# Optimization experiments

Measured on AMD Instinct MI355X. Metric: run time of the kernel, lower is better.

## Reference

```python
import jax, jax.numpy as jnp
import numpy as np

E, H, F, N, B = 512, 8, 2048, 1024, 4
HD = E // H


def setup_inputs() -> dict:
    key = jax.random.key(0)
    ks = jax.random.split(key, 20)
    s = 0.02
    return {
        "node_inputs": jax.random.normal(ks[0], (N, B, E), jnp.float32),
        "parent_mask": jax.random.uniform(ks[1], (B, N, N), jnp.float32),
        "hidden": jax.random.bernoulli(ks[2], 0.5, (B, N, N)),
        "pad_mask": jax.random.bernoulli(ks[3], 0.1, (B, N)),
        "Wp": jax.random.normal(ks[4], (H, E), jnp.float32) * s,
        "bp": jnp.zeros((H,), jnp.float32),
        "Wc": jax.random.normal(ks[5], (H, E), jnp.float32) * s,
        "bc": jnp.zeros((H,), jnp.float32),
        "Wqkv": jax.random.normal(ks[6], (3 * E, E), jnp.float32) * s,
        "bqkv": jnp.zeros((3 * E,), jnp.float32),
        "Wo": jax.random.normal(ks[7], (E, E), jnp.float32) * s,
        "bo": jnp.zeros((E,), jnp.float32),
        "W1": jax.random.normal(ks[8], (F, E), jnp.float32) * s,
        "b1": jnp.zeros((F,), jnp.float32),
        "W2": jax.random.normal(ks[9], (E, F), jnp.float32) * s,
        "b2": jnp.zeros((E,), jnp.float32),
        "ln1_g": jnp.ones((E,), jnp.float32),
        "ln1_b": jnp.zeros((E,), jnp.float32),
        "ln2_g": jnp.ones((E,), jnp.float32),
        "ln2_b": jnp.zeros((E,), jnp.float32),
    }


def _layer_norm(x, g, b, eps=1e-5):
    m = jnp.mean(x, axis=-1, keepdims=True)
    v = jnp.mean((x - m) ** 2, axis=-1, keepdims=True)
    return (x - m) * jax.lax.rsqrt(v + eps) * g + b


def reference(node_inputs, parent_mask, hidden, pad_mask, Wp, bp, Wc, bc,
              Wqkv, bqkv, Wo, bo, W1, b1, W2, b2, ln1_g, ln1_b, ln2_g, ln2_b):
    x = node_inputs  # (N, B, E), seq-first like nn.TransformerEncoderLayer
    # parent/child per-head biases: Linear(E->H), permuted to (B, H, N)
    pbias = jnp.transpose(x @ Wp.T + bp, (1, 2, 0))
    cbias = jnp.transpose(x @ Wc.T + bc, (1, 2, 0))
    # additive attention bias (B, H, N, N)
    am = (jnp.swapaxes(parent_mask, 1, 2)[:, None] * pbias[..., None]
          + parent_mask[:, None] * cbias[..., None])
    am = jnp.where(hidden[:, None], -jnp.inf, am)
    # multi-head self-attention
    qkv = x @ Wqkv.T + bqkv  # (N, B, 3E)
    q, k, v = jnp.split(qkv, 3, axis=-1)

    def heads(t):  # (N, B, E) -> (B, H, N, HD)
        return jnp.transpose(t.reshape(N, B, H, HD), (1, 2, 0, 3))

    q, k, v = heads(q), heads(k), heads(v)
    scores = jnp.einsum("bhqd,bhkd->bhqk", q, k) / jnp.sqrt(jnp.float32(HD)) + am
    scores = jnp.where(pad_mask[:, None, None, :], -jnp.inf, scores)
    attn = jax.nn.softmax(scores, axis=-1)
    ctx = jnp.einsum("bhqk,bhkd->bhqd", attn, v)  # (B, H, N, HD)
    ctx = jnp.transpose(ctx, (2, 0, 1, 3)).reshape(N, B, E)
    attn_out = ctx @ Wo.T + bo
    # post-norm transformer encoder layer (dropout=0, relu activation)
    y = _layer_norm(x + attn_out, ln1_g, ln1_b)
    ff = jax.nn.relu(y @ W1.T + b1) @ W2.T + b2
    return _layer_norm(y + ff, ln2_g, ln2_b)
```

## Files before the change

### kernel.cpp

```cpp
#include <hip/hip_runtime.h>
#include <hip/hip_bf16.h>
#include <stdint.h>

using bf16 = __hip_bfloat16;

typedef __bf16 bf16x8 __attribute__((ext_vector_type(8)));
typedef float  f32x4  __attribute__((ext_vector_type(4)));

__device__ __forceinline__ float bflo(uint32_t u) { return __uint_as_float(u << 16); }
__device__ __forceinline__ float bfhi(uint32_t u) { return __uint_as_float(u & 0xffff0000u); }

__device__ __forceinline__ void load8(const bf16* p, float* f) {
  uint4 u = *(const uint4*)p;
  f[0] = bflo(u.x); f[1] = bfhi(u.x);
  f[2] = bflo(u.y); f[3] = bfhi(u.y);
  f[4] = bflo(u.z); f[5] = bfhi(u.z);
  f[6] = bflo(u.w); f[7] = bfhi(u.w);
}
__device__ __forceinline__ void load8(const float* p, float* f) {
  float4 a = *(const float4*)p, b = *(const float4*)(p + 4);
  f[0] = a.x; f[1] = a.y; f[2] = a.z; f[3] = a.w;
  f[4] = b.x; f[5] = b.y; f[6] = b.z; f[7] = b.w;
}
__device__ __forceinline__ void store1(float* o, float v) { *o = v; }
__device__ __forceinline__ void store1(bf16* o, float v) { *o = __float2bfloat16(v); }
__device__ __forceinline__ uint32_t bfbits(float x) {
  bf16 v = __float2bfloat16(x);
  return (uint32_t)*(uint16_t*)&v;
}

typedef const uint32_t __attribute__((address_space(1)))* gp_t;
typedef uint32_t __attribute__((address_space(3)))* lp_t;
__device__ __forceinline__ void gload16(const void* g, void* l) {
  __builtin_amdgcn_global_load_lds((gp_t)g, (lp_t)l, 16, 0, 0);
}

__global__ __launch_bounds__(256)
void prologue(const float* __restrict__ pm, const int* __restrict__ hid,
              const int* __restrict__ padm, uint32_t* __restrict__ mout,
              const float* __restrict__ x, const float* __restrict__ Wqkv,
              const float* __restrict__ Wo, const float* __restrict__ W1,
              const float* __restrict__ W2, bf16* __restrict__ xb,
              bf16* __restrict__ wq, bf16* __restrict__ wob,
              bf16* __restrict__ w1b, bf16* __restrict__ w2b,
              const float* __restrict__ bqkv, const float* __restrict__ bp,
              const float* __restrict__ bc, const float* __restrict__ Wp,
              const float* __restrict__ Wc, float* __restrict__ bias_ext)
{
  __shared__ float tileT[128][65];
  const int blk = blockIdx.x, t = threadIdx.x;
  if (blk < 512) {
    const int k0 = (blk & 7) * 128, q0 = ((blk >> 3) & 15) * 64, b = blk >> 7;
    const size_t pb = (size_t)b << 20;
#pragma unroll
    for (int i = 0; i < 32; ++i) {
      int idx = t + i * 256;
      int r = idx >> 6, c = idx & 63;
      tileT[r][c] = pm[pb + (size_t)(k0 + r) * 1024 + q0 + c];
    }
    __syncthreads();
#pragma unroll
    for (int i = 0; i < 32; ++i) {
      int idx = t + i * 256;
      int q = idx >> 7, k = idx & 127;
      size_t src = pb + (size_t)(q0 + q) * 1024 + k0 + k;
      int msk = hid[src] | padm[b * 1024 + k0 + k];
      uint32_t u = 0xFFFFFFFFu;
      if (!msk) u = (bfbits(tileT[k][q]) << 16) | bfbits(pm[src]);
      mout[src] = u;
    }
  } else if (blk < 3072) {
    size_t j = ((size_t)(blk - 512) * 256 + t) * 8;
    const float* s; bf16* o; size_t off;
    if      (j < 2097152) { s = x;    o = xb;  off = j; }
    else if (j < 2883584) { s = Wqkv; o = wq;  off = j - 2097152; }
    else if (j < 3145728) { s = Wo;   o = wob; off = j - 2883584; }
    else if (j < 4194304) { s = W1;   o = w1b; off = j - 3145728; }
    else                  { s = W2;   o = w2b; off = j - 4194304; }
    float f[8];
    load8(s + off, f);
    uint4 u;
    u.x = (bfbits(f[1]) << 16) | bfbits(f[0]);
    u.y = (bfbits(f[3]) << 16) | bfbits(f[2]);
    u.z = (bfbits(f[5]) << 16) | bfbits(f[4]);
    u.w = (bfbits(f[7]) << 16) | bfbits(f[6]);
    *(uint4*)(o + off) = u;
  } else {
    int sb = blk - 3072;
    if (sb < 2) {
      int j = (sb * 256 + t) * 8;
      if (j < 4096) {
        float f[8]; load8(Wp + j, f);
#pragma unroll
        for (int i = 0; i < 8; ++i) wq[(size_t)1536 * 512 + j + i] = __float2bfloat16(f[i]);
      }
    } else if (sb < 4) {
      int j = ((sb - 2) * 256 + t) * 8;
      if (j < 4096) {
        float f[8]; load8(Wc + j, f);
#pragma unroll
        for (int i = 0; i < 8; ++i) wq[(size_t)1544 * 512 + j + i] = __float2bfloat16(f[i]);
      }
    } else {
      int j = t * 8;
#pragma unroll
      for (int i = 0; i < 8; ++i) {
        int cc = j + i;
        if (cc < 1664) {
          float v = 0.f;
          if (cc < 1536) v = bqkv[cc];
          else if (cc < 1544) v = bp[cc - 1536];
          else if (cc < 1552) v = bc[cc - 1544];
          bias_ext[cc] = v;
        }
      }
    }
  }
}

template<int MODE, int BN>
__global__ __launch_bounds__(256)
void gemm_bt(const bf16* __restrict__ A, const bf16* __restrict__ W,
             const float* __restrict__ bias, bf16* __restrict__ outb,
             float* __restrict__ outf, int M, int Nout, int K, int kLen)
{
  constexpr int NT = BN / 32;
  __shared__ bf16 As[128 * 64];
  __shared__ bf16 Bs[BN * 64];
  const int t = threadIdx.x, lane = t & 63, wave = t >> 6;
  const int m0 = blockIdx.y * 128, n0 = blockIdx.x * BN;
  const int kOff = blockIdx.z * kLen;
  if (MODE == 3) outf += (size_t)blockIdx.z * M * Nout;
  const int wr = wave >> 1, wc = wave & 1;
  const int frow = lane & 15, ksel = (lane >> 4) * 8;
  f32x4 acc[4 * NT] = {};
  const bf16* Ab = A + (size_t)m0 * K;
  const bf16* Wb = W + (size_t)n0 * K;

  for (int k0 = kOff; k0 < kOff + kLen; k0 += 64) {
    __syncthreads();
#pragma unroll
    for (int i = 0; i < 4; ++i) {
      int ib = i * 256 + wave * 64;
      int idx = ib + lane;
      gload16(Ab + (size_t)(idx >> 3) * K + k0 + (idx & 7) * 8, As + ib * 8);
    }
#pragma unroll
    for (int i = 0; i < BN / 32; ++i) {
      int ib = i * 256 + wave * 64;
      int idx = ib + lane;
      gload16(Wb + (size_t)(idx >> 3) * K + k0 + (idx & 7) * 8, Bs + ib * 8);
    }
    __syncthreads();
#pragma unroll
    for (int kk = 0; kk < 64; kk += 32) {
      bf16x8 af[4], bf_[NT];
#pragma unroll
      for (int mt = 0; mt < 4; ++mt)
        af[mt] = *(const bf16x8*)(As + (wr * 64 + mt * 16 + frow) * 64 + kk + ksel);
#pragma unroll
      for (int nt = 0; nt < NT; ++nt)
        bf_[nt] = *(const bf16x8*)(Bs + (wc * (BN / 2) + nt * 16 + frow) * 64 + kk + ksel);
#pragma unroll
      for (int mt = 0; mt < 4; ++mt)
#pragma unroll
        for (int nt = 0; nt < NT; ++nt)
          acc[mt * NT + nt] = __builtin_amdgcn_mfma_f32_16x16x32_bf16(
              af[mt], bf_[nt], acc[mt * NT + nt], 0, 0, 0);
    }
  }
  const int rb = (lane >> 4) * 4, cb = lane & 15;
#pragma unroll
  for (int mt = 0; mt < 4; ++mt)
#pragma unroll
    for (int nt = 0; nt < NT; ++nt) {
      f32x4 a = acc[mt * NT + nt];
#pragma unroll
      for (int r = 0; r < 4; ++r) {
        int row = m0 + wr * 64 + mt * 16 + rb + r;
        int col = n0 + wc * (BN / 2) + nt * 16 + cb;
        if (MODE == 3) {
          outf[(size_t)row * Nout + col] = a[r];
        } else {
          float v = a[r] + bias[col];
          if (MODE == 1) v = fmaxf(v, 0.f);
          if (MODE == 2) {
            if (col >= 1552) continue;
            int n = row >> 2, b = row & 3;
            if (col >= 1536) {
              int j = col - 1536;
              int hh = j & 7;
              outf[(j < 8 ? 0 : 32768) + (b * 8 + hh) * 1024 + n] = v;
            } else {
              int which = col >> 9, hh = (col >> 6) & 7, d = col & 63;
              if (which == 0) v *= 0.125f;
              size_t idx;
              if (which == 2)
                idx = (((size_t)(64 + b * 8 + hh)) << 16) + (size_t)d * 1024 + n;
              else
                idx = (((size_t)(which * 32 + b * 8 + hh)) << 16) + (size_t)n * 64 + d;
              outb[idx] = __float2bfloat16(v);
            }
          } else {
            outb[(size_t)row * Nout + col] = __float2bfloat16(v);
          }
        }
      }
    }
}

__global__ __launch_bounds__(256, 3)
void attn_mfma(const bf16* __restrict__ qkv, const float* __restrict__ pbw,
               const float* __restrict__ cbw, const uint32_t* __restrict__ mpk,
               bf16* __restrict__ opart, float2* __restrict__ mlout)
{
  __shared__ bf16 Kt[128 * 64];
  __shared__ bf16 Vt[64 * 128];
  __shared__ bf16 Ps[4][16][136];
  const int t = threadIdx.x, lane = t & 63, wave = t >> 6;
  const int g = lane >> 4, c = lane & 15;
  const int h = blockIdx.y, b = blockIdx.z >> 1, half = blockIdx.z & 1;
  const int q0 = blockIdx.x * 64 + wave * 16;
  const size_t bh = (size_t)b * 8 + h;
  const bf16* Qp = qkv + (bh << 16);
  const bf16* Kp = qkv + ((32 + bh) << 16);
  const bf16* Vg = qkv + ((64 + bh) << 16);

  bf16x8 qa0 = *(const bf16x8*)(Qp + (size_t)(q0 + c) * 64 + g * 8);
  bf16x8 qa1 = *(const bf16x8*)(Qp + (size_t)(q0 + c) * 64 + 32 + g * 8);

  const float pbq = pbw[bh * 1024 + q0 + c];
  const float cbq = cbw[bh * 1024 + q0 + c];
  const uint32_t* mrp = mpk + (((size_t)b * 1024 + q0 + c) << 10);

  f32x4 oacc[4] = {{0,0,0,0},{0,0,0,0},{0,0,0,0},{0,0,0,0}};
  float m = -1e30f, l = 0.f;

  for (int kt = 0; kt < 4; ++kt) {
    const int k0 = half * 512 + kt * 128;
    __syncthreads();
#pragma unroll
    for (int i = 0; i < 4; ++i) {
      int ib = i * 256 + wave * 64;
      int idx = ib + lane;
      int r = idx >> 3, p = idx & 7;
      gload16(Kp + (size_t)(k0 + r) * 64 + ((p ^ (r & 7)) * 8), Kt + ib * 8);
    }
#pragma unroll
    for (int i = 0; i < 4; ++i) {
      int ib = i * 256 + wave * 64;
      int idx = ib + lane;
      int d = idx >> 4, p = idx & 15;
      gload16(Vg + (size_t)d * 1024 + k0 + ((p ^ (d & 15)) * 8), Vt + ib * 8);
    }
    uint4 mu[8];
#pragma unroll
    for (int nt = 0; nt < 8; ++nt)
      mu[nt] = *(const uint4*)(mrp + k0 + nt * 16 + 4 * g);
    __syncthreads();
    f32x4 sacc[8];
#pragma unroll
    for (int nt = 0; nt < 8; ++nt) {
      f32x4 z = {0.f,0.f,0.f,0.f};
      int r = nt * 16 + c;
      bf16x8 k0f = *(const bf16x8*)(Kt + r * 64 + (( g      ^ (c & 7)) * 8));
      bf16x8 k1f = *(const bf16x8*)(Kt + r * 64 + (((4 + g) ^ (c & 7)) * 8));
      z = __builtin_amdgcn_mfma_f32_16x16x32_bf16(k0f, qa0, z, 0, 0, 0);
      z = __builtin_amdgcn_mfma_f32_16x16x32_bf16(k1f, qa1, z, 0, 0, 0);
      sacc[nt] = z;
    }
    float mx = -1e30f;
#pragma unroll
    for (int nt = 0; nt < 8; ++nt) {
      uint32_t uu[4] = {mu[nt].x, mu[nt].y, mu[nt].z, mu[nt].w};
#pragma unroll
      for (int r = 0; r < 4; ++r) {
        float s = sacc[nt][r] + bfhi(uu[r]) * pbq + bflo(uu[r]) * cbq;
        s = (uu[r] == 0xFFFFFFFFu) ? -1e30f : s;
        sacc[nt][r] = s;
        mx = fmaxf(mx, s);
      }
    }
    mx = fmaxf(mx, __shfl_xor(mx, 16));
    mx = fmaxf(mx, __shfl_xor(mx, 32));
    const float newm = fmaxf(m, mx);
    const float al = __expf(m - newm);
    float ps = 0.f;
#pragma unroll
    for (int nt = 0; nt < 8; ++nt) {
      float p0 = (sacc[nt][0] <= -1e29f) ? 0.f : __expf(sacc[nt][0] - newm);
      float p1 = (sacc[nt][1] <= -1e29f) ? 0.f : __expf(sacc[nt][1] - newm);
      float p2 = (sacc[nt][2] <= -1e29f) ? 0.f : __expf(sacc[nt][2] - newm);
      float p3 = (sacc[nt][3] <= -1e29f) ? 0.f : __expf(sacc[nt][3] - newm);
      ps += (p0 + p1) + (p2 + p3);
      uint2 w;
      w.x = (bfbits(p1) << 16) | bfbits(p0);
      w.y = (bfbits(p3) << 16) | bfbits(p2);
      *(uint2*)&Ps[wave][c][nt * 16 + 4 * g] = w;
    }
    ps += __shfl_xor(ps, 16);
    ps += __shfl_xor(ps, 32);
    l = l * al + ps;
    m = newm;
#pragma unroll
    for (int dt = 0; dt < 4; ++dt) {
      oacc[dt][0] *= al; oacc[dt][1] *= al;
      oacc[dt][2] *= al; oacc[dt][3] *= al;
    }
#pragma unroll
    for (int dt = 0; dt < 4; ++dt) {
      int row = dt * 16 + c;
#pragma unroll
      for (int kc = 0; kc < 4; ++kc) {
        bf16x8 vf = *(const bf16x8*)(Vt + row * 128 + (((kc * 4 + g) ^ c) * 8));
        bf16x8 pf = *(const bf16x8*)&Ps[wave][c][kc * 32 + g * 8];
        oacc[dt] = __builtin_amdgcn_mfma_f32_16x16x32_bf16(vf, pf, oacc[dt], 0, 0, 0);
      }
    }
  }
  const int qg = q0 + c;
  const size_t prow = ((size_t)(half * 32) + bh) * 1024 + qg;
#pragma unroll
  for (int dt = 0; dt < 4; ++dt)
#pragma unroll
    for (int rg = 0; rg < 4; ++rg)
      opart[prow * 64 + dt * 16 + 4 * g + rg] = __float2bfloat16(oacc[dt][rg]);
  if (g == 0) mlout[prow] = make_float2(m, l);
}

__global__ __launch_bounds__(256)
void attn_reduce(const bf16* __restrict__ opart, const float2* __restrict__ ml,
                 bf16* __restrict__ ctxo)
{
  const int idx = blockIdx.x * 256 + threadIdx.x;
  const int row = idx >> 3, seg = (idx & 7) * 8;
  float o0[8], o1[8];
  load8(opart + (size_t)row * 64 + seg, o0);
  load8(opart + (size_t)(row + 32768) * 64 + seg, o1);
  const float2 ml0 = ml[row], ml1 = ml[row + 32768];
  const float mst = fmaxf(ml0.x, ml1.x);
  const float w0 = __expf(ml0.x - mst), w1 = __expf(ml1.x - mst);
  const float denom = ml0.y * w0 + ml1.y * w1;
  const float inv = (denom > 0.f) ? 1.f / denom : 0.f;
  const int bh = row >> 10, q = row & 1023;
  const int b = bh >> 3, h = bh & 7;
  bf16* out = ctxo + ((size_t)q * 4 + b) * 512 + h * 64 + seg;
#pragma unroll
  for (int j = 0; j < 8; ++j)
    out[j] = __float2bfloat16((o0[j] * w0 + o1[j] * w1) * inv);
}

template<typename TA, typename TO>
__global__ __launch_bounds__(256)
void ln_res2(const TA* __restrict__ a, const float* __restrict__ p0,
             const float* __restrict__ p1, const float* __restrict__ bias,
             const float* __restrict__ g, const float* __restrict__ be,
             TO* __restrict__ out)
{
  const int wave = threadIdx.x >> 6, lane = threadIdx.x & 63;
  const int m = blockIdx.x * 4 + wave;
  const size_t base = (size_t)m * 512 + lane * 8;
  float va[8], f0[8], f1[8], bb[8];
  load8(a + base, va);
  load8(p0 + base, f0);
  load8(p1 + base, f1);
  load8(bias + lane * 8, bb);
  float v[8], s = 0.f;
#pragma unroll
  for (int j = 0; j < 8; ++j) { v[j] = va[j] + f0[j] + f1[j] + bb[j]; s += v[j]; }
#pragma unroll
  for (int off = 32; off; off >>= 1) s += __shfl_xor(s, off);
  const float mean = s * (1.f / 512.f);
  float q = 0.f;
#pragma unroll
  for (int j = 0; j < 8; ++j) { float d = v[j] - mean; q += d * d; }
#pragma unroll
  for (int off = 32; off; off >>= 1) q += __shfl_xor(q, off);
  const float rs = rsqrtf(q * (1.f / 512.f) + 1e-5f);
  float gv[8], bv[8];
  load8(g + lane * 8, gv);
  load8(be + lane * 8, bv);
#pragma unroll
  for (int j = 0; j < 8; ++j)
    store1(out + base + j, (v[j] - mean) * rs * gv[j] + bv[j]);
}

extern "C" void kernel_launch(void* const* d_in, const int* in_sizes, int n_in,
                              void* d_out, int out_size, void* d_ws, size_t ws_size,
                              hipStream_t stream)
{
  (void)in_sizes; (void)n_in; (void)out_size; (void)ws_size;
  const float* x    = (const float*)d_in[0];
  const float* pm   = (const float*)d_in[1];
  const int*   hid  = (const int*)d_in[2];
  const int*   padm = (const int*)d_in[3];
  const float* Wp   = (const float*)d_in[4];
  const float* bp   = (const float*)d_in[5];
  const float* Wc   = (const float*)d_in[6];
  const float* bc   = (const float*)d_in[7];
  const float* Wqkv = (const float*)d_in[8];
  const float* bqkv = (const float*)d_in[9];
  const float* Wo   = (const float*)d_in[10];
  const float* bo   = (const float*)d_in[11];
  const float* W1   = (const float*)d_in[12];
  const float* b1   = (const float*)d_in[13];
  const float* W2   = (const float*)d_in[14];
  const float* b2   = (const float*)d_in[15];
  const float* g1   = (const float*)d_in[16];
  const float* be1  = (const float*)d_in[17];
  const float* g2   = (const float*)d_in[18];
  const float* be2  = (const float*)d_in[19];

  char* ws = (char*)d_ws;
  bf16*     qkvb  = (bf16*)    (ws);
  float*    pbo   = (float*)   (ws + 12582912);
  float*    cbo   = (float*)   (ws + 12713984);
  uint32_t* mpk   = (uint32_t*)(ws + 12845056);
  bf16*     ctx   = (bf16*)    (ws + 29622272);
  float*    part  = (float*)   (ws);
  bf16*     ff1   = (bf16*)    (ws + 16777216);
  bf16*     y     = (bf16*)    (ws + 33816576);
  bf16*     xb    = (bf16*)    (ws + 38010880);
  bf16*     wqkvb = (bf16*)    (ws + 42205184);
  bf16*     wob   = (bf16*)    (ws + 43909120);
  bf16*     w1b   = (bf16*)    (ws + 44433408);
  bf16*     w2b   = (bf16*)    (ws + 46530560);
  float*    bext  = (float*)   (ws + 48627712);
  bf16*     opart = (bf16*)    (ws + 48634368);
  float2*   mlb   = (float2*)  (ws + 57022976);
  float*    part1 = part + (size_t)4096 * 512;

  prologue<<<3077, 256, 0, stream>>>(pm, hid, padm, mpk, x, Wqkv, Wo, W1, W2,
                                     xb, wqkvb, wob, w1b, w2b,
                                     bqkv, bp, bc, Wp, Wc, bext);
  gemm_bt<2, 128><<<dim3(13, 32), 256, 0, stream>>>(xb, wqkvb, bext, qkvb, pbo, 4096, 1664, 512, 512);
  attn_mfma<<<dim3(16, 8, 8), 256, 0, stream>>>(qkvb, pbo, cbo, mpk, opart, mlb);
  attn_reduce<<<1024, 256, 0, stream>>>(opart, mlb, ctx);
  gemm_bt<3, 64><<<dim3(8, 32, 2), 256, 0, stream>>>(ctx, wob, nullptr, nullptr, part, 4096, 512, 512, 256);
  ln_res2<float, bf16><<<1024, 256, 0, stream>>>(x, part, part1, bo, g1, be1, y);
  gemm_bt<1, 128><<<dim3(16, 32), 256, 0, stream>>>(y, w1b, b1, ff1, nullptr, 4096, 2048, 512, 512);
  gemm_bt<3, 64><<<dim3(8, 32, 2), 256, 0, stream>>>(ff1, w2b, nullptr, nullptr, part, 4096, 512, 2048, 1024);
  ln_res2<bf16, float><<<1024, 256, 0, stream>>>(y, part, part1, b2, g2, be2, (float*)d_out);
}
```

Baseline: 272.0 us.

## Co-schedule mask packing with QKV GEMM in one heterogeneous kernel

Moves the parent-mask transpose and pack work out of the prologue into a combined kernel with the QKV projection GEMM. Blocks 0-415 run the GEMM and the remaining 512 blocks build the packed mask. The aim is to overlap the memory-bound mask pass with the compute-bound GEMM, so neither leaves the GPU idle on its own. This adds a shared-memory union and a larger per-block footprint, which may lower GEMM occupancy.

```diff
diff --git a/kernel.cpp b/kernel.cpp
--- a/kernel.cpp
+++ b/kernel.cpp
@@ -36,9 +36,7 @@
 }
 
 __global__ __launch_bounds__(256)
-void prologue(const float* __restrict__ pm, const int* __restrict__ hid,
-              const int* __restrict__ padm, uint32_t* __restrict__ mout,
-              const float* __restrict__ x, const float* __restrict__ Wqkv,
+void cvt_prep(const float* __restrict__ x, const float* __restrict__ Wqkv,
               const float* __restrict__ Wo, const float* __restrict__ W1,
               const float* __restrict__ W2, bf16* __restrict__ xb,
               bf16* __restrict__ wq, bf16* __restrict__ wob,
@@ -47,30 +45,9 @@
               const float* __restrict__ bc, const float* __restrict__ Wp,
               const float* __restrict__ Wc, float* __restrict__ bias_ext)
 {
-  __shared__ float tileT[128][65];
   const int blk = blockIdx.x, t = threadIdx.x;
-  if (blk < 512) {
-    const int k0 = (blk & 7) * 128, q0 = ((blk >> 3) & 15) * 64, b = blk >> 7;
-    const size_t pb = (size_t)b << 20;
-#pragma unroll
-    for (int i = 0; i < 32; ++i) {
-      int idx = t + i * 256;
-      int r = idx >> 6, c = idx & 63;
-      tileT[r][c] = pm[pb + (size_t)(k0 + r) * 1024 + q0 + c];
-    }
-    __syncthreads();
-#pragma unroll
-    for (int i = 0; i < 32; ++i) {
-      int idx = t + i * 256;
-      int q = idx >> 7, k = idx & 127;
-      size_t src = pb + (size_t)(q0 + q) * 1024 + k0 + k;
-      int msk = hid[src] | padm[b * 1024 + k0 + k];
-      uint32_t u = 0xFFFFFFFFu;
-      if (!msk) u = (bfbits(tileT[k][q]) << 16) | bfbits(pm[src]);
-      mout[src] = u;
-    }
-  } else if (blk < 3072) {
-    size_t j = ((size_t)(blk - 512) * 256 + t) * 8;
+  if (blk < 2560) {
+    size_t j = ((size_t)blk * 256 + t) * 8;
     const float* s; bf16* o; size_t off;
     if      (j < 2097152) { s = x;    o = xb;  off = j; }
     else if (j < 2883584) { s = Wqkv; o = wq;  off = j - 2097152; }
@@ -86,7 +63,7 @@
     u.w = (bfbits(f[7]) << 16) | bfbits(f[6]);
     *(uint4*)(o + off) = u;
   } else {
-    int sb = blk - 3072;
+    int sb = blk - 2560;
     if (sb < 2) {
       int j = (sb * 256 + t) * 8;
       if (j < 4096) {
@@ -114,6 +91,111 @@
           bias_ext[cc] = v;
         }
       }
+    }
+  }
+}
+
+__global__ __launch_bounds__(256)
+void qkv_mask(const bf16* __restrict__ A, const bf16* __restrict__ W,
+              const float* __restrict__ bias, bf16* __restrict__ outb,
+              float* __restrict__ outf,
+              const float* __restrict__ pm, const int* __restrict__ hid,
+              const int* __restrict__ padm, uint32_t* __restrict__ mout)
+{
+  __shared__ char smem[33280];
+  const int blk = blockIdx.x, t = threadIdx.x;
+  if (blk < 416) {
+    bf16* As = (bf16*)smem;
+    bf16* Bs = (bf16*)(smem + 16384);
+    const int lane = t & 63, wave = t >> 6;
+    const int m0 = (blk / 13) * 128, n0 = (blk % 13) * 128;
+    const int wr = wave >> 1, wc = wave & 1;
+    const int frow = lane & 15, ksel = (lane >> 4) * 8;
+    f32x4 acc[16] = {};
+    const bf16* Ab = A + (size_t)m0 * 512;
+    const bf16* Wb = W + (size_t)n0 * 512;
+    for (int k0 = 0; k0 < 512; k0 += 64) {
+      __syncthreads();
+#pragma unroll
+      for (int i = 0; i < 4; ++i) {
+        int ib = i * 256 + wave * 64;
+        int idx = ib + lane;
+        gload16(Ab + (size_t)(idx >> 3) * 512 + k0 + (idx & 7) * 8, As + ib * 8);
+      }
+#pragma unroll
+      for (int i = 0; i < 4; ++i) {
+        int ib = i * 256 + wave * 64;
+        int idx = ib + lane;
+        gload16(Wb + (size_t)(idx >> 3) * 512 + k0 + (idx & 7) * 8, Bs + ib * 8);
+      }
+      __syncthreads();
+#pragma unroll
+      for (int kk = 0; kk < 64; kk += 32) {
+        bf16x8 af[4], bf_[4];
+#pragma unroll
+        for (int mt = 0; mt < 4; ++mt)
+          af[mt] = *(const bf16x8*)(As + (wr * 64 + mt * 16 + frow) * 64 + kk + ksel);
+#pragma unroll
+        for (int nt = 0; nt < 4; ++nt)
+          bf_[nt] = *(const bf16x8*)(Bs + (wc * 64 + nt * 16 + frow) * 64 + kk + ksel);
+#pragma unroll
+        for (int mt = 0; mt < 4; ++mt)
+#pragma unroll
+          for (int nt = 0; nt < 4; ++nt)
+            acc[mt * 4 + nt] = __builtin_amdgcn_mfma_f32_16x16x32_bf16(
+                af[mt], bf_[nt], acc[mt * 4 + nt], 0, 0, 0);
+      }
+    }
+    const int rb = (lane >> 4) * 4, cb = lane & 15;
+#pragma unroll
+    for (int mt = 0; mt < 4; ++mt)
+#pragma unroll
+      for (int nt = 0; nt < 4; ++nt) {
+        f32x4 a = acc[mt * 4 + nt];
+#pragma unroll
+        for (int r = 0; r < 4; ++r) {
+          int row = m0 + wr * 64 + mt * 16 + rb + r;
+          int col = n0 + wc * 64 + nt * 16 + cb;
+          if (col >= 1552) continue;
+          float v = a[r] + bias[col];
+          int n = row >> 2, b = row & 3;
+          if (col >= 1536) {
+            int j = col - 1536;
+            int hh = j & 7;
+            outf[(j < 8 ? 0 : 32768) + (b * 8 + hh) * 1024 + n] = v;
+          } else {
+            int which = col >> 9, hh = (col >> 6) & 7, d = col & 63;
+            if (which == 0) v *= 0.125f;
+            size_t idx;
+            if (which == 2)
+              idx = (((size_t)(64 + b * 8 + hh)) << 16) + (size_t)d * 1024 + n;
+            else
+              idx = (((size_t)(which * 32 + b * 8 + hh)) << 16) + (size_t)n * 64 + d;
+            outb[idx] = __float2bfloat16(v);
+          }
+        }
+      }
+  } else {
+    float (*tileT)[65] = (float(*)[65])smem;
+    const int mb = blk - 416;
+    const int k0 = (mb & 7) * 128, q0 = ((mb >> 3) & 15) * 64, b = mb >> 7;
+    const size_t pb = (size_t)b << 20;
+#pragma unroll
+    for (int i = 0; i < 32; ++i) {
+      int idx = t + i * 256;
+      int r = idx >> 6, c = idx & 63;
+      tileT[r][c] = pm[pb + (size_t)(k0 + r) * 1024 + q0 + c];
+    }
+    __syncthreads();
+#pragma unroll
+    for (int i = 0; i < 32; ++i) {
+      int idx = t + i * 256;
+      int q = idx >> 7, k = idx & 127;
+      size_t src = pb + (size_t)(q0 + q) * 1024 + k0 + k;
+      int msk = hid[src] | padm[b * 1024 + k0 + k];
+      uint32_t u = 0xFFFFFFFFu;
+      if (!msk) u = (bfbits(tileT[k][q]) << 16) | bfbits(pm[src]);
+      mout[src] = u;
     }
   }
 }
@@ -184,26 +266,7 @@
         } else {
           float v = a[r] + bias[col];
           if (MODE == 1) v = fmaxf(v, 0.f);
-          if (MODE == 2) {
-            if (col >= 1552) continue;
-            int n = row >> 2, b = row & 3;
-            if (col >= 1536) {
-              int j = col - 1536;
-              int hh = j & 7;
-              outf[(j < 8 ? 0 : 32768) + (b * 8 + hh) * 1024 + n] = v;
-            } else {
-              int which = col >> 9, hh = (col >> 6) & 7, d = col & 63;
-              if (which == 0) v *= 0.125f;
-              size_t idx;
-              if (which == 2)
-                idx = (((size_t)(64 + b * 8 + hh)) << 16) + (size_t)d * 1024 + n;
-              else
-                idx = (((size_t)(which * 32 + b * 8 + hh)) << 16) + (size_t)n * 64 + d;
-              outb[idx] = __float2bfloat16(v);
-            }
-          } else {
-            outb[(size_t)row * Nout + col] = __float2bfloat16(v);
-          }
+          outb[(size_t)row * Nout + col] = __float2bfloat16(v);
         }
       }
     }
@@ -430,10 +493,10 @@
   float2*   mlb   = (float2*)  (ws + 57022976);
   float*    part1 = part + (size_t)4096 * 512;
 
-  prologue<<<3077, 256, 0, stream>>>(pm, hid, padm, mpk, x, Wqkv, Wo, W1, W2,
-                                     xb, wqkvb, wob, w1b, w2b,
+  cvt_prep<<<2565, 256, 0, stream>>>(x, Wqkv, Wo, W1, W2, xb, wqkvb, wob, w1b, w2b,
                                      bqkv, bp, bc, Wp, Wc, bext);
-  gemm_bt<2, 128><<<dim3(13, 32), 256, 0, stream>>>(xb, wqkvb, bext, qkvb, pbo, 4096, 1664, 512, 512);
+  qkv_mask<<<928, 256, 0, stream>>>(xb, wqkvb, bext, qkvb, pbo,
+                                    pm, hid, padm, mpk);
   attn_mfma<<<dim3(16, 8, 8), 256, 0, stream>>>(qkvb, pbo, cbo, mpk, opart, mlb);
   attn_reduce<<<1024, 256, 0, stream>>>(opart, mlb, ctx);
   gemm_bt<3, 64><<<dim3(8, 32, 2), 256, 0, stream>>>(ctx, wob, nullptr, nullptr, part, 4096, 512, 512, 256);
```

Result: no change. 271.0 us (-0.4%).
